# Performance work log

Measured on AMD Instinct MI355X. Metric: run time of the kernel, lower is better.

## Reference

```python
import jax, jax.numpy as jnp
import numpy as np

HEADS = 16
KEY = 64          # key_size == size_per_head
NEG = 1e10


def setup_inputs() -> dict:
    key = jax.random.key(0)
    k1, k2, k3, k4, k5, k6 = jax.random.split(key, 6)
    B, S, D = 2, 2048, 1024
    scale = 1.0 / np.sqrt(D).astype(np.float32)
    return {
        "q": jax.random.normal(k1, (B, S, D), jnp.float32),
        "k": jax.random.normal(k2, (B, S, D), jnp.float32),
        "v": jax.random.normal(k3, (B, S, D), jnp.float32),
        "Wq": jax.random.normal(k4, (D, HEADS * KEY), jnp.float32) * scale,
        "Wk": jax.random.normal(k5, (D, HEADS * KEY), jnp.float32) * scale,
        "Wv": jax.random.normal(k6, (D, HEADS * KEY), jnp.float32) * scale,
    }


def reference(q, k, v, Wq, Wk, Wv):
    B, Sq, _ = q.shape
    Skv = k.shape[1]
    # projections (no bias), split heads: (B, S, H*Dh) -> (B, H, S, Dh)
    qw = (q @ Wq).reshape(B, Sq, HEADS, KEY).transpose(0, 2, 1, 3)
    kw = (k @ Wk).reshape(B, Skv, HEADS, KEY).transpose(0, 2, 1, 3)
    vw = (v @ Wv).reshape(B, Skv, HEADS, KEY).transpose(0, 2, 1, 3)
    inv_sqrt_d = jnp.asarray(1.0 / np.sqrt(KEY), dtype=qw.dtype)
    a = jnp.einsum("bhqd,bhkd->bhqk", qw, kw) * inv_sqrt_d  # (B,H,Sq,Skv)
    # mask_right=True: causal additive mask a - (1 - tril)*1e10
    causal = jnp.tril(jnp.ones((Sq, Skv), dtype=a.dtype))
    a = a - (1.0 - causal) * jnp.asarray(NEG, dtype=a.dtype)
    a = jax.nn.softmax(a, axis=-1)
    o = jnp.einsum("bhqk,bhkd->bhqd", a, vw)  # (B,H,Sq,Dh)
    o = o.transpose(0, 2, 1, 3).reshape(B, Sq, HEADS * KEY)
    return o
```

## Files before the change

kernel.cpp:

```cpp
#include <hip/hip_runtime.h>
#include <hip/hip_bf16.h>

#define HEADS 16
#define KEY   64
#define BB    2
#define SS    2048
#define DD    1024
#define NCOL  1024

typedef __attribute__((ext_vector_type(8))) short bf16x8;
typedef __attribute__((ext_vector_type(4))) float f32x4;
typedef __attribute__((ext_vector_type(8))) unsigned short u16x8;

typedef const __attribute__((address_space(1))) void* gas_ptr;
typedef __attribute__((address_space(3))) void* las_ptr;

__device__ __forceinline__ void gload_lds16(const void* g, void* l) {
  __builtin_amdgcn_global_load_lds((gas_ptr)g, (las_ptr)l, 16, 0, 0);
}

__device__ __forceinline__ unsigned short f2bf(float f) {
  unsigned u = __builtin_bit_cast(unsigned, f);
  u = (u + 0x7FFFu + ((u >> 16) & 1u)) >> 16;
  return (unsigned short)u;
}

__device__ __forceinline__ float bf2f(unsigned short u) {
  return __builtin_bit_cast(float, (unsigned)u << 16);
}

__device__ __forceinline__ unsigned cvtpk(float lo, float hi) {
  unsigned r;
  asm("v_cvt_pk_bf16_f32 %0, %1, %2" : "=v"(r) : "v"(lo), "v"(hi));
  return r;
}

__device__ __forceinline__ f32x4 mfma_bf16(bf16x8 a, bf16x8 b, f32x4 c) {
  return __builtin_amdgcn_mfma_f32_16x16x32_bf16(a, b, c, 0, 0, 0);
}

__global__ __launch_bounds__(256) void cvt3(const float* __restrict__ q,
                                            const float* __restrict__ k,
                                            const float* __restrict__ v,
                                            unsigned short* __restrict__ qo,
                                            unsigned short* __restrict__ ko,
                                            unsigned short* __restrict__ vo) {
  const float* in = blockIdx.y == 0 ? q : (blockIdx.y == 1 ? k : v);
  unsigned short* out = blockIdx.y == 0 ? qo : (blockIdx.y == 1 ? ko : vo);
  int i = blockIdx.x * blockDim.x + threadIdx.x;
  const float4* p = reinterpret_cast<const float4*>(in) + (size_t)i * 2;
  float4 a = p[0], b = p[1];
  u16x8 o;
  o[0] = f2bf(a.x); o[1] = f2bf(a.y); o[2] = f2bf(a.z); o[3] = f2bf(a.w);
  o[4] = f2bf(b.x); o[5] = f2bf(b.y); o[6] = f2bf(b.z); o[7] = f2bf(b.w);
  reinterpret_cast<u16x8*>(out)[i] = o;
}

__global__ __launch_bounds__(1024) void trw(const float* __restrict__ W0,
                                            const float* __restrict__ W1,
                                            const float* __restrict__ W2,
                                            unsigned short* __restrict__ T0,
                                            unsigned short* __restrict__ T1,
                                            unsigned short* __restrict__ T2) {
  const float* W = blockIdx.z == 0 ? W0 : (blockIdx.z == 1 ? W1 : W2);
  unsigned short* T = blockIdx.z == 0 ? T0 : (blockIdx.z == 1 ? T1 : T2);
  __shared__ float tile[32][33];
  int tx = threadIdx.x, ty = threadIdx.y;
  tile[ty][tx] = W[(size_t)(blockIdx.y * 32 + ty) * DD + blockIdx.x * 32 + tx];
  __syncthreads();
  T[(size_t)(blockIdx.x * 32 + ty) * DD + blockIdx.y * 32 + tx] = f2bf(tile[tx][ty]);
}

template <int MODE>
__global__ __launch_bounds__(256) void gemm_proj(const unsigned short* __restrict__ X,
                                                 const unsigned short* __restrict__ WT,
                                                 unsigned short* __restrict__ O) {
  __shared__ __align__(16) unsigned short As[128 * 32];
  __shared__ __align__(16) unsigned short Bs[128 * 32];

  const int tid = threadIdx.x;
  const int w = tid >> 6, l = tid & 63;
  const int m0 = blockIdx.x * 128, n0 = blockIdx.y * 128;
  const int wm = (w >> 1) * 64, wn = (w & 1) * 64;
  const int g = l >> 4, c = l & 15;

  const int srow = tid >> 2;
  const int scol = 8 * ((tid & 3) ^ ((tid >> 3) & 3));
  const int kb = ((g ^ ((c >> 1) & 3)) << 3);

  f32x4 acc[4][4] = {};

  for (int k0 = 0; k0 < DD; k0 += 32) {
#pragma unroll
    for (int i = 0; i < 2; ++i) {
      gload_lds16(X + (size_t)(m0 + i * 64 + srow) * DD + k0 + scol,
                  (char*)As + i * 4096 + w * 1024);
      gload_lds16(WT + (size_t)(n0 + i * 64 + srow) * DD + k0 + scol,
                  (char*)Bs + i * 4096 + w * 1024);
    }
    __syncthreads();
    bf16x8 af[4], bfr[4];
#pragma unroll
    for (int mi = 0; mi < 4; mi++)
      af[mi] = *reinterpret_cast<const bf16x8*>(&As[(wm + mi * 16 + c) * 32 + kb]);
#pragma unroll
    for (int ni = 0; ni < 4; ni++)
      bfr[ni] = *reinterpret_cast<const bf16x8*>(&Bs[(wn + ni * 16 + c) * 32 + kb]);
#pragma unroll
    for (int mi = 0; mi < 4; mi++)
#pragma unroll
      for (int ni = 0; ni < 4; ni++) {
        if constexpr (MODE == 2)
          acc[mi][ni] = mfma_bf16(bfr[ni], af[mi], acc[mi][ni]);
        else
          acc[mi][ni] = mfma_bf16(af[mi], bfr[ni], acc[mi][ni]);
      }
    __syncthreads();
  }

  if constexpr (MODE != 2) {
    const float osc = (MODE == 0) ? 0.180336880f : 1.0f;
#pragma unroll
    for (int mi = 0; mi < 4; mi++)
#pragma unroll
      for (int ni = 0; ni < 4; ni++)
#pragma unroll
        for (int r = 0; r < 4; r++) {
          int row = m0 + wm + mi * 16 + g * 4 + r;
          int col = n0 + wn + ni * 16 + c;
          O[(size_t)row * NCOL + col] = f2bf(acc[mi][ni][r] * osc);
        }
  } else {
#pragma unroll
    for (int mi = 0; mi < 4; mi++) {
      const int mbase = m0 + wm + mi * 16;
      const int bb_ = mbase >> 11;
      const int s = (mbase & 2047) + c;
#pragma unroll
      for (int ni = 0; ni < 4; ni++)
#pragma unroll
        for (int r = 0; r < 4; r++) {
          int n = n0 + wn + ni * 16 + g * 4 + r;
          O[((size_t)(bb_ * 1024 + n) << 11) + s] = f2bf(acc[mi][ni][r]);
        }
    }
  }
}

__global__ __launch_bounds__(256) void attn(const unsigned short* __restrict__ qw,
                                            const unsigned short* __restrict__ kw,
                                            const unsigned short* __restrict__ vt,
                                            unsigned short* __restrict__ opart,
                                            float* __restrict__ mlb,
                                            float* __restrict__ out) {
  __shared__ __align__(16) char smem[40960];
  char* KsRaw = smem;
  char* VsRaw = smem + 16384;
  unsigned short* Pl = (unsigned short*)(smem + 32768);
  float* Osc = (float*)smem;

  const int tid = threadIdx.x, w = tid >> 6, l = tid & 63;
  const int g = l >> 4, c = l & 15;
  const int x = blockIdx.x, h = blockIdx.y, b = blockIdx.z;

  int qt, ci, nchunks;
  if (x < 8)       { qt = x;                ci = 0;            nchunks = 1; }
  else if (x < 24) { qt = 8 + ((x - 8) >> 1);  ci = (x - 8) & 1;  nchunks = 2; }
  else if (x < 48) { qt = 16 + (x - 24) / 3;   ci = (x - 24) % 3; nchunks = 3; }
  else             { qt = 24 + ((x - 48) >> 2); ci = (x - 48) & 3; nchunks = 4; }
  const int nt = qt + 1;
  const int t_begin = ci * 8;
  const int t_end = min(t_begin + 8, nt);
  const int q0 = qt * 64;
  const int cid = (b * HEADS + h) * 80 + x;

  const int qrow = q0 + w * 16 + c;
  const size_t qbase = ((size_t)(b * SS) + qrow) * NCOL + h * KEY;
  bf16x8 qf[2];
  qf[0] = *reinterpret_cast<const bf16x8*>(qw + qbase + g * 8);
  qf[1] = *reinterpret_cast<const bf16x8*>(qw + qbase + g * 8 + 32);

  f32x4 oacc[4] = {};
  float m = -1e30f, lsum = 0.f;

  const int krow = w * 8 + (l >> 3);
  const int kcsw = 8 * ((l & 7) ^ (l >> 3));
  const size_t kbase = (size_t)(b * SS) * NCOL + h * KEY;
  const size_t vbase = (size_t)(b * HEADS + h) * KEY * SS;

  {
    const int kv0 = t_begin * 64;
#pragma unroll
    for (int j = 0; j < 2; ++j) {
      gload_lds16(kw + kbase + (size_t)(kv0 + j * 32 + krow) * NCOL + kcsw,
                  KsRaw + j * 4096 + w * 1024);
      gload_lds16(vt + vbase + (size_t)(j * 32 + krow) * SS + kv0 + kcsw,
                  VsRaw + j * 4096 + w * 1024);
    }
  }
  __syncthreads();

  unsigned short* Pw = Pl + w * 1024;
  int cur = 0;
  for (int it = t_begin; it < t_end; ++it) {
    if (it + 1 < t_end) {
      const int kv1 = (it + 1) * 64, nx = cur ^ 1;
#pragma unroll
      for (int j = 0; j < 2; ++j) {
        gload_lds16(kw + kbase + (size_t)(kv1 + j * 32 + krow) * NCOL + kcsw,
                    KsRaw + nx * 8192 + j * 4096 + w * 1024);
        gload_lds16(vt + vbase + (size_t)(j * 32 + krow) * SS + kv1 + kcsw,
                    VsRaw + nx * 8192 + j * 4096 + w * 1024);
      }
    }
    const unsigned short* Kc = (const unsigned short*)(KsRaw + cur * 8192);
    const unsigned short* Vc = (const unsigned short*)(VsRaw + cur * 8192);

    f32x4 sacc[4] = {};
    __builtin_amdgcn_s_setprio(1);
#pragma unroll
    for (int t = 0; t < 4; t++)
#pragma unroll
      for (int ks = 0; ks < 2; ks++) {
        const int off = ((g | (ks << 2)) ^ (c & 7)) << 3;
        bf16x8 kf = *reinterpret_cast<const bf16x8*>(&Kc[(t * 16 + c) * 64 + off]);
        sacc[t] = mfma_bf16(kf, qf[ks], sacc[t]);
      }
    __builtin_amdgcn_s_setprio(0);

    float p[4][4];
#pragma unroll
    for (int t = 0; t < 4; t++)
#pragma unroll
      for (int r = 0; r < 4; r++) p[t][r] = sacc[t][r];
    if (it == nt - 1) {
#pragma unroll
      for (int t = 0; t < 4; t++)
#pragma unroll
        for (int r = 0; r < 4; r++)
          if (it * 64 + 16 * t + 4 * g + r > qrow) p[t][r] = -3.0e38f;
    }
    float tm[4];
#pragma unroll
    for (int t = 0; t < 4; t++)
      tm[t] = fmaxf(fmaxf(p[t][0], p[t][1]), fmaxf(p[t][2], p[t][3]));
    float pm = fmaxf(fmaxf(tm[0], tm[1]), fmaxf(tm[2], tm[3]));
    pm = fmaxf(pm, __shfl_xor(pm, 16));
    pm = fmaxf(pm, __shfl_xor(pm, 32));
    if (__ballot(pm > m + 8.0f)) {
      float mn = fmaxf(m, pm);
      float al = exp2f(m - mn);
      m = mn; lsum *= al;
#pragma unroll
      for (int t = 0; t < 4; t++) oacc[t] *= al;
    }
    float ts[4];
#pragma unroll
    for (int t = 0; t < 4; t++) {
#pragma unroll
      for (int r = 0; r < 4; r++) p[t][r] = exp2f(p[t][r] - m);
      ts[t] = (p[t][0] + p[t][1]) + (p[t][2] + p[t][3]);
    }
    float rs = (ts[0] + ts[1]) + (ts[2] + ts[3]);
    rs += __shfl_xor(rs, 16);
    rs += __shfl_xor(rs, 32);
    lsum += rs;

#pragma unroll
    for (int t = 0; t < 4; t++)
#pragma unroll
      for (int rr = 0; rr < 2; rr++) {
        unsigned pk = cvtpk(p[t][2 * rr], p[t][2 * rr + 1]);
        int col = 16 * t + 4 * g + 2 * rr;
        *reinterpret_cast<unsigned*>(&Pw[c * 64 + (col ^ ((c & 7) << 3))]) = pk;
      }
    bf16x8 pf[2];
#pragma unroll
    for (int ks = 0; ks < 2; ks++)
      pf[ks] = *reinterpret_cast<const bf16x8*>(
          &Pw[c * 64 + (((g | (ks << 2)) ^ (c & 7)) << 3)]);

    __builtin_amdgcn_s_setprio(1);
#pragma unroll
    for (int t = 0; t < 4; t++)
#pragma unroll
      for (int ks = 0; ks < 2; ks++) {
        const int off = ((g | (ks << 2)) ^ (c & 7)) << 3;
        bf16x8 vf = *reinterpret_cast<const bf16x8*>(&Vc[(t * 16 + c) * 64 + off]);
        oacc[t] = mfma_bf16(vf, pf[ks], oacc[t]);
      }
    __builtin_amdgcn_s_setprio(0);
    __syncthreads();
    cur ^= 1;
  }

  const float inv = (nchunks == 1) ? 1.0f / lsum : 1.0f;
#pragma unroll
  for (int t = 0; t < 4; t++)
#pragma unroll
    for (int rr = 0; rr < 2; rr++) {
      float2 v2 = make_float2(oacc[t][2 * rr] * inv, oacc[t][2 * rr + 1] * inv);
      *reinterpret_cast<float2*>(&Osc[(w * 16 + c) * 72 + 16 * t + 4 * g + 2 * rr]) = v2;
    }
  if (nchunks > 1 && l < 16) {
    float* mlp = mlb + (size_t)cid * 128 + w * 16 + c;
    mlp[0] = m;
    mlp[64] = lsum;
  }
  __syncthreads();

  const int row = tid >> 2, sg = (tid & 3) << 4;
  if (nchunks == 1) {
    float* op = out + ((size_t)(b * SS) + q0 + row) * NCOL + h * KEY + sg;
#pragma unroll
    for (int kk = 0; kk < 4; kk++)
      reinterpret_cast<float4*>(op)[kk] =
          *reinterpret_cast<const float4*>(&Osc[row * 72 + sg + kk * 4]);
  } else {
    unsigned* pp = reinterpret_cast<unsigned*>(opart + (size_t)cid * 4096 + row * 64 + sg);
#pragma unroll
    for (int e = 0; e < 8; e++)
      pp[e] = cvtpk(Osc[row * 72 + sg + 2 * e], Osc[row * 72 + sg + 2 * e + 1]);
  }
}

__global__ __launch_bounds__(256) void attn_reduce(const unsigned short* __restrict__ opart,
                                                   const float* __restrict__ mlb,
                                                   float* __restrict__ out) {
  const int qt = 8 + blockIdx.x, h = blockIdx.y, b = blockIdx.z;
  int base, nc;
  if (qt < 16)      { base = 8 + 2 * (qt - 8);   nc = 2; }
  else if (qt < 24) { base = 24 + 3 * (qt - 16); nc = 3; }
  else              { base = 48 + 4 * (qt - 24); nc = 4; }
  const int cid0 = (b * HEADS + h) * 80 + base;
  const int row = threadIdx.x >> 2, sg = (threadIdx.x & 3) << 4;

  float mv[4], lv[4], M = -1e30f;
#pragma unroll
  for (int i = 0; i < 4; i++)
    if (i < nc) {
      mv[i] = mlb[(size_t)(cid0 + i) * 128 + row];
      lv[i] = mlb[(size_t)(cid0 + i) * 128 + 64 + row];
      M = fmaxf(M, mv[i]);
    }
  float L = 0.f, acc[16];
#pragma unroll
  for (int e = 0; e < 16; e++) acc[e] = 0.f;
#pragma unroll
  for (int i = 0; i < 4; i++)
    if (i < nc) {
      float s = exp2f(mv[i] - M);
      L += s * lv[i];
      const u16x8* pp = reinterpret_cast<const u16x8*>(
          opart + (size_t)(cid0 + i) * 4096 + row * 64 + sg);
      u16x8 o0 = pp[0], o1 = pp[1];
#pragma unroll
      for (int e = 0; e < 8; e++) {
        acc[e]     += s * bf2f(o0[e]);
        acc[8 + e] += s * bf2f(o1[e]);
      }
    }
  const float inv = 1.0f / L;
  float* op = out + ((size_t)(b * SS) + qt * 64 + row) * NCOL + h * KEY + sg;
#pragma unroll
  for (int kk = 0; kk < 4; kk++) {
    float4 v;
    v.x = acc[4 * kk] * inv;     v.y = acc[4 * kk + 1] * inv;
    v.z = acc[4 * kk + 2] * inv; v.w = acc[4 * kk + 3] * inv;
    reinterpret_cast<float4*>(op)[kk] = v;
  }
}

extern "C" void kernel_launch(void* const* d_in, const int* in_sizes, int n_in,
                              void* d_out, int out_size, void* d_ws, size_t ws_size,
                              hipStream_t stream) {
  const float* q  = (const float*)d_in[0];
  const float* k  = (const float*)d_in[1];
  const float* v  = (const float*)d_in[2];
  const float* Wq = (const float*)d_in[3];
  const float* Wk = (const float*)d_in[4];
  const float* Wv = (const float*)d_in[5];
  float* out = (float*)d_out;

  unsigned short* ws  = (unsigned short*)d_ws;
  const size_t ACT = (size_t)4 * 1024 * 1024;
  const size_t WEL = (size_t)1024 * 1024;
  unsigned short* qbf = ws;
  unsigned short* kbf = qbf + ACT;
  unsigned short* vbf = kbf + ACT;
  unsigned short* WqT = vbf + ACT;
  unsigned short* WkT = WqT + WEL;
  unsigned short* WvT = WkT + WEL;
  unsigned short* qwp = WvT + WEL;
  unsigned short* kwp = qwp + ACT;
  unsigned short* vt  = kwp + ACT;
  unsigned short* opart = kbf;
  float*          mlb   = (float*)WvT;

  cvt3<<<dim3(2048, 3), 256, 0, stream>>>(q, k, v, qbf, kbf, vbf);
  trw<<<dim3(32, 32, 3), dim3(32, 32), 0, stream>>>(Wq, Wk, Wv, WqT, WkT, WvT);
  gemm_proj<0><<<dim3(32, 8), 256, 0, stream>>>(qbf, WqT, qwp);
  gemm_proj<1><<<dim3(32, 8), 256, 0, stream>>>(kbf, WkT, kwp);
  gemm_proj<2><<<dim3(32, 8), 256, 0, stream>>>(vbf, WvT, vt);
  attn<<<dim3(80, 16, 2), 256, 0, stream>>>(qwp, kwp, vt, opart, mlb, out);
  attn_reduce<<<dim3(24, 16, 2), 256, 0, stream>>>(opart, mlb, out);
}
```

Measured before the change: 227.9 us.

## Merge three projection GEMMs into one launch with K-tile of 64

Replaces the three separate projection GEMM launches with one launch that picks Q/K/V operands from blockIdx.z, so all 768 tiles run concurrently instead of 256 per launch. The K step per iteration doubles from 32 to 64 with a matching 8-way XOR swizzle, halving the number of barrier pairs per tile at the cost of double the LDS. MFMA blocks are wrapped with s_setprio. Mode becomes a runtime branch instead of a template parameter, which adds minor divergence-free branching.

New measurement: 207.4 us. 9.0% less time.

```diff
diff --git a/kernel.cpp b/kernel.cpp
--- a/kernel.cpp
+++ b/kernel.cpp
@@ -71,55 +71,80 @@
   T[(size_t)(blockIdx.x * 32 + ty) * DD + blockIdx.y * 32 + tx] = f2bf(tile[tx][ty]);
 }
 
-template <int MODE>
-__global__ __launch_bounds__(256) void gemm_proj(const unsigned short* __restrict__ X,
-                                                 const unsigned short* __restrict__ WT,
-                                                 unsigned short* __restrict__ O) {
-  __shared__ __align__(16) unsigned short As[128 * 32];
-  __shared__ __align__(16) unsigned short Bs[128 * 32];
+__global__ __launch_bounds__(256) void gemm_proj3(
+    const unsigned short* __restrict__ X0, const unsigned short* __restrict__ X1,
+    const unsigned short* __restrict__ X2,
+    const unsigned short* __restrict__ W0, const unsigned short* __restrict__ W1,
+    const unsigned short* __restrict__ W2,
+    unsigned short* __restrict__ O0, unsigned short* __restrict__ O1,
+    unsigned short* __restrict__ O2) {
+  const int mode = blockIdx.z;
+  const unsigned short* X; const unsigned short* WT; unsigned short* O;
+  if (mode == 0)      { X = X0; WT = W0; O = O0; }
+  else if (mode == 1) { X = X1; WT = W1; O = O1; }
+  else                { X = X2; WT = W2; O = O2; }
+
+  __shared__ __align__(16) unsigned short As[128 * 64];
+  __shared__ __align__(16) unsigned short Bs[128 * 64];
 
   const int tid = threadIdx.x;
-  const int w = tid >> 6, l = tid & 63;
+  const int w = tid >> 6;
+  const int l = tid & 63;
   const int m0 = blockIdx.x * 128, n0 = blockIdx.y * 128;
   const int wm = (w >> 1) * 64, wn = (w & 1) * 64;
   const int g = l >> 4, c = l & 15;
 
-  const int srow = tid >> 2;
-  const int scol = 8 * ((tid & 3) ^ ((tid >> 3) & 3));
-  const int kb = ((g ^ ((c >> 1) & 3)) << 3);
+  const int srow = tid >> 3;
+  const int scol = 8 * ((tid & 7) ^ ((tid >> 3) & 7));
 
   f32x4 acc[4][4] = {};
 
-  for (int k0 = 0; k0 < DD; k0 += 32) {
-#pragma unroll
-    for (int i = 0; i < 2; ++i) {
-      gload_lds16(X + (size_t)(m0 + i * 64 + srow) * DD + k0 + scol,
+  for (int k0 = 0; k0 < DD; k0 += 64) {
+#pragma unroll
+    for (int i = 0; i < 4; ++i) {
+      gload_lds16(X + (size_t)(m0 + i * 32 + srow) * DD + k0 + scol,
                   (char*)As + i * 4096 + w * 1024);
-      gload_lds16(WT + (size_t)(n0 + i * 64 + srow) * DD + k0 + scol,
+      gload_lds16(WT + (size_t)(n0 + i * 32 + srow) * DD + k0 + scol,
                   (char*)Bs + i * 4096 + w * 1024);
     }
     __syncthreads();
-    bf16x8 af[4], bfr[4];
-#pragma unroll
-    for (int mi = 0; mi < 4; mi++)
-      af[mi] = *reinterpret_cast<const bf16x8*>(&As[(wm + mi * 16 + c) * 32 + kb]);
-#pragma unroll
-    for (int ni = 0; ni < 4; ni++)
-      bfr[ni] = *reinterpret_cast<const bf16x8*>(&Bs[(wn + ni * 16 + c) * 32 + kb]);
-#pragma unroll
-    for (int mi = 0; mi < 4; mi++)
-#pragma unroll
-      for (int ni = 0; ni < 4; ni++) {
-        if constexpr (MODE == 2)
-          acc[mi][ni] = mfma_bf16(bfr[ni], af[mi], acc[mi][ni]);
-        else
-          acc[mi][ni] = mfma_bf16(af[mi], bfr[ni], acc[mi][ni]);
-      }
+    bf16x8 af[2][4], bfr[2][4];
+#pragma unroll
+    for (int kk = 0; kk < 2; kk++) {
+      const int kb = (((kk << 2) | g) ^ (c & 7)) << 3;
+#pragma unroll
+      for (int mi = 0; mi < 4; mi++)
+        af[kk][mi] = *reinterpret_cast<const bf16x8*>(&As[(wm + mi * 16 + c) * 64 + kb]);
+#pragma unroll
+      for (int ni = 0; ni < 4; ni++)
+        bfr[kk][ni] = *reinterpret_cast<const bf16x8*>(&Bs[(wn + ni * 16 + c) * 64 + kb]);
+    }
+    if (mode == 2) {
+      __builtin_amdgcn_s_setprio(1);
+#pragma unroll
+      for (int kk = 0; kk < 2; kk++)
+#pragma unroll
+        for (int mi = 0; mi < 4; mi++)
+#pragma unroll
+          for (int ni = 0; ni < 4; ni++)
+            acc[mi][ni] = mfma_bf16(bfr[kk][ni], af[kk][mi], acc[mi][ni]);
+      __builtin_amdgcn_s_setprio(0);
+    } else {
+      __builtin_amdgcn_s_setprio(1);
+#pragma unroll
+      for (int kk = 0; kk < 2; kk++)
+#pragma unroll
+        for (int mi = 0; mi < 4; mi++)
+#pragma unroll
+          for (int ni = 0; ni < 4; ni++)
+            acc[mi][ni] = mfma_bf16(af[kk][mi], bfr[kk][ni], acc[mi][ni]);
+      __builtin_amdgcn_s_setprio(0);
+    }
     __syncthreads();
   }
 
-  if constexpr (MODE != 2) {
-    const float osc = (MODE == 0) ? 0.180336880f : 1.0f;
+  if (mode != 2) {
+    const float osc = (mode == 0) ? 0.180336880f : 1.0f;
 #pragma unroll
     for (int mi = 0; mi < 4; mi++)
 #pragma unroll
@@ -399,9 +424,8 @@
 
   cvt3<<<dim3(2048, 3), 256, 0, stream>>>(q, k, v, qbf, kbf, vbf);
   trw<<<dim3(32, 32, 3), dim3(32, 32), 0, stream>>>(Wq, Wk, Wv, WqT, WkT, WvT);
-  gemm_proj<0><<<dim3(32, 8), 256, 0, stream>>>(qbf, WqT, qwp);
-  gemm_proj<1><<<dim3(32, 8), 256, 0, stream>>>(kbf, WkT, kwp);
-  gemm_proj<2><<<dim3(32, 8), 256, 0, stream>>>(vbf, WvT, vt);
+  gemm_proj3<<<dim3(32, 8, 3), 256, 0, stream>>>(qbf, kbf, vbf, WqT, WkT, WvT,
+                                                 qwp, kwp, vt);
   attn<<<dim3(80, 16, 2), 256, 0, stream>>>(qwp, kwp, vt, opart, mlb, out);
   attn_reduce<<<dim3(24, 16, 2), 256, 0, stream>>>(opart, mlb, out);
 }
```
